# Performance work log

Measured on AMD Instinct MI355X. Metric: run time of the kernel, lower is better.

## Reference

```python
import jax, jax.numpy as jnp
import numpy as np

B, S, H = 8, 128, 768  # batch, seq_len, hidden (guide==vis)
EPS = 1e-12


def setup_inputs() -> dict:
    key = jax.random.key(0)
    ks = jax.random.split(key, 5)
    return {
        "seq_hiddens_x": jax.random.normal(ks[0], (B, S, H), jnp.float32),
        "seq_hiddens_y": jax.random.normal(ks[1], (B, S, H), jnp.float32),
        "cat_W": jax.random.normal(ks[2], (H, 2 * H), jnp.float32) * 0.02,
        "cat_b": jnp.zeros((H,), jnp.float32),
        "beta": jnp.zeros((H,), jnp.float32),
        "gamma": jnp.ones((H,), jnp.float32),
        "beta_W": jax.random.normal(ks[3], (H, H), jnp.float32) * 0.02,
        "gamma_W": jax.random.normal(ks[4], (H, H), jnp.float32) * 0.02,
    }


def reference(seq_hiddens_x, seq_hiddens_y, cat_W, cat_b, beta, gamma, beta_W, gamma_W):
    s = seq_hiddens_x.shape[1]
    # upper_reg2seq: flatten upper-triangular (i<=j) pairs, row-major
    ii, jj = np.triu_indices(s)
    guide = seq_hiddens_x[:, ii, :]    # (B, P, H)
    visible = seq_hiddens_y[:, jj, :]  # (B, P, H)

    # 'cat' branch: relu(Linear([guide; visible]))
    cat_pre = jax.nn.relu(
        jnp.einsum('bph,oh->bpo', jnp.concatenate([guide, visible], axis=-1), cat_W) + cat_b
    )

    # 'cln' branch: conditional LayerNorm(visible, cond=guide)
    # NOTE: original code uses std = (var + eps)**2 (not sqrt) -- replicated faithfully.
    b = jnp.einsum('bph,oh->bpo', guide, beta_W) + beta
    g = jnp.einsum('bph,oh->bpo', guide, gamma_W) + gamma
    mean = jnp.mean(visible, axis=-1, keepdims=True)
    cen = visible - mean
    var = jnp.mean(cen * cen, axis=-1, keepdims=True)
    std = (var + EPS) ** 2
    cln_pre = cen / std * g + b

    return (cat_pre + cln_pre) / 2.0
```

## Files before the change

kernel.cpp:

```cpp
#include <hip/hip_runtime.h>
#include <hip/hip_bf16.h>
#include <math.h>
#include <stdint.h>

#define S_LEN 128
#define H_DIM 768
#define B_DIM 8
#define NPAIR 8256
#define MROWS 1024
#define NTOT  3072
#define EPSC  1e-12f
#define CHUNK 8

typedef __bf16 bf16x8 __attribute__((ext_vector_type(8)));
typedef float  f32x4  __attribute__((ext_vector_type(4)));

static __device__ __forceinline__ unsigned short f2bf(float f) {
  union { float f; unsigned u; } a; a.f = f;
  unsigned u = a.u;
  u += 0x7fffu + ((u >> 16) & 1u);
  return (unsigned short)(u >> 16);
}
static __device__ __forceinline__ float bf2f(unsigned short s) {
  union { unsigned u; float f; } a; a.u = ((unsigned)s) << 16;
  return a.f;
}
static __device__ __forceinline__ float4 ld_bf4(const unsigned short* p) {
  ushort4 u = *(const ushort4*)p;
  float4 f; f.x = bf2f(u.x); f.y = bf2f(u.y); f.z = bf2f(u.z); f.w = bf2f(u.w);
  return f;
}

__global__ __launch_bounds__(256) void prep(const float* __restrict__ x,
                                            const float* __restrict__ y,
                                            const float* __restrict__ catW,
                                            const float* __restrict__ betaW,
                                            const float* __restrict__ gammaW,
                                            unsigned short* __restrict__ Xb,
                                            unsigned short* __restrict__ Yb,
                                            unsigned short* __restrict__ Wb,
                                            float* __restrict__ mean,
                                            float* __restrict__ inv) {
  const int bid = blockIdx.x;
  const int tid = threadIdx.x;
  if (bid < MROWS) {
    const int row = bid;
    float s = 0.f, s2 = 0.f;
    if (tid < 192) {
      const int o = tid * 4;
      float4 vx = *(const float4*)(x + (size_t)row * H_DIM + o);
      float4 vy = *(const float4*)(y + (size_t)row * H_DIM + o);
      ushort4 ox; ox.x = f2bf(vx.x); ox.y = f2bf(vx.y); ox.z = f2bf(vx.z); ox.w = f2bf(vx.w);
      ushort4 oy; oy.x = f2bf(vy.x); oy.y = f2bf(vy.y); oy.z = f2bf(vy.z); oy.w = f2bf(vy.w);
      *(ushort4*)(Xb + (size_t)row * H_DIM + o) = ox;
      *(ushort4*)(Yb + (size_t)row * H_DIM + o) = oy;
      s  = vy.x + vy.y + vy.z + vy.w;
      s2 = vy.x * vy.x + vy.y * vy.y + vy.z * vy.z + vy.w * vy.w;
    }
    for (int off = 32; off > 0; off >>= 1) { s += __shfl_down(s, off); s2 += __shfl_down(s2, off); }
    __shared__ float ls[4], ls2[4];
    if ((tid & 63) == 0) { ls[tid >> 6] = s; ls2[tid >> 6] = s2; }
    __syncthreads();
    if (tid == 0) {
      float S1 = ls[0] + ls[1] + ls[2] + ls[3];
      float S2 = ls2[0] + ls2[1] + ls2[2] + ls2[3];
      float m = S1 / H_DIM;
      float var = S2 / H_DIM - m * m;
      float st = var + EPSC;
      mean[row] = m;
      inv[row] = 1.0f / (st * st);
    }
  } else {
    int idx = (bid - MROWS) * 256 + tid;
    int e = idx * 4;
    int n = e / H_DIM, k = e % H_DIM;
    const float* src;
    if      (n < 768)  src = catW   + (size_t)n * 1536 + k;
    else if (n < 1536) src = betaW  + (size_t)(n - 768) * 768 + k;
    else if (n < 2304) src = gammaW + (size_t)(n - 1536) * 768 + k;
    else               src = catW   + (size_t)(n - 2304) * 1536 + 768 + k;
    float4 v = *(const float4*)src;
    ushort4 o; o.x = f2bf(v.x); o.y = f2bf(v.y); o.z = f2bf(v.z); o.w = f2bf(v.w);
    *(ushort4*)(Wb + e) = o;
  }
}

__device__ __forceinline__ void gload_lds16(const void* g, void* l) {
  __builtin_amdgcn_global_load_lds(
      (const __attribute__((address_space(1))) unsigned int*)(uintptr_t)g,
      (__attribute__((address_space(3))) unsigned int*)(uintptr_t)l,
      16, 0, 0);
}

__global__ __launch_bounds__(256) void gemm_bt(const unsigned short* __restrict__ Xb,
                                               const unsigned short* __restrict__ Yb,
                                               const unsigned short* __restrict__ Wb,
                                               unsigned short* __restrict__ P) {
  __shared__ unsigned short As[64 * 32];
  __shared__ unsigned short Bs[64 * 32];
  const int m0 = blockIdx.x * 64;
  const int n0 = blockIdx.y * 64;
  const unsigned short* A = (n0 < 2304) ? Xb : Yb;
  const unsigned short* Arow = A + (size_t)m0 * H_DIM;
  const unsigned short* Brow = Wb + (size_t)n0 * H_DIM;

  const int tid  = threadIdx.x;
  const int lane = tid & 63;
  const int wave = tid >> 6;
  const int wm = (wave >> 1) * 32;
  const int wn = (wave & 1) * 32;
  const int quad = lane >> 4;
  const int r    = lane & 15;

  const int ar = tid >> 2;
  const int ac = (tid & 3) * 8;

  f32x4 acc[2][2] = {};

  for (int k0 = 0; k0 < H_DIM; k0 += 32) {
    gload_lds16(Arow + (size_t)ar * H_DIM + k0 + ac, &As[tid * 8]);
    gload_lds16(Brow + (size_t)ar * H_DIM + k0 + ac, &Bs[tid * 8]);
    __syncthreads();

    bf16x8 af[2], bfr[2];
#pragma unroll
    for (int mi = 0; mi < 2; ++mi)
      af[mi] = *(const bf16x8*)&As[(wm + mi * 16 + r) * 32 + quad * 8];
#pragma unroll
    for (int ni = 0; ni < 2; ++ni)
      bfr[ni] = *(const bf16x8*)&Bs[(wn + ni * 16 + r) * 32 + quad * 8];
#pragma unroll
    for (int mi = 0; mi < 2; ++mi)
#pragma unroll
      for (int ni = 0; ni < 2; ++ni)
        acc[mi][ni] = __builtin_amdgcn_mfma_f32_16x16x32_bf16(af[mi], bfr[ni], acc[mi][ni], 0, 0, 0);
    __syncthreads();
  }

#pragma unroll
  for (int mi = 0; mi < 2; ++mi) {
#pragma unroll
    for (int ni = 0; ni < 2; ++ni) {
      const int row = m0 + wm + mi * 16 + quad * 4;
      const int col = n0 + wn + ni * 16 + r;
#pragma unroll
      for (int reg = 0; reg < 4; ++reg)
        P[(size_t)(row + reg) * NTOT + col] = f2bf(acc[mi][ni][reg]);
    }
  }
}

__global__ __launch_bounds__(192) void epilogue(const unsigned short* __restrict__ P,
                                                const float* __restrict__ Yf,
                                                const float* __restrict__ mean,
                                                const float* __restrict__ inv,
                                                const float* __restrict__ cat_b,
                                                const float* __restrict__ beta,
                                                const float* __restrict__ gamma,
                                                float* __restrict__ out) {
  const int b  = blockIdx.y;
  const int p0 = blockIdx.x * CHUNK;
  const int o  = threadIdx.x * 4;

  int i = (int)((257.0 - sqrt(257.0 * 257.0 - 8.0 * (double)p0)) * 0.5);
  if (i < 0) i = 0;
  if (i > S_LEN - 1) i = S_LEN - 1;
  while ((i + 1) * (256 - i) / 2 <= p0) ++i;
  while (i * (257 - i) / 2 > p0) --i;

  float4 cb = *(const float4*)(cat_b + o);
  float4 be = *(const float4*)(beta + o);
  float4 ga = *(const float4*)(gamma + o);

  size_t ri = (size_t)(b * S_LEN + i) * NTOT;
  float4 ax = ld_bf4(P + ri + o);
  float4 bx = ld_bf4(P + ri + 768 + o);
  float4 gx = ld_bf4(P + ri + 1536 + o);

#pragma unroll
  for (int t = 0; t < CHUNK; ++t) {
    const int p = p0 + t;
    bool moved = false;
    while ((i + 1) * (256 - i) / 2 <= p) { ++i; moved = true; }
    if (moved) {
      ri = (size_t)(b * S_LEN + i) * NTOT;
      ax = ld_bf4(P + ri + o);
      bx = ld_bf4(P + ri + 768 + o);
      gx = ld_bf4(P + ri + 1536 + o);
    }
    const int j = i + (p - i * (257 - i) / 2);
    const int rowj = b * S_LEN + j;
    float4 ay = ld_bf4(P + (size_t)rowj * NTOT + 2304 + o);
    float4 yv = *(const float4*)(Yf + (size_t)rowj * H_DIM + o);
    const float m  = mean[rowj];
    const float iv = inv[rowj];
    float4 rr;
    rr.x = 0.5f * (fmaxf(ax.x + ay.x + cb.x, 0.f) + (yv.x - m) * iv * (gx.x + ga.x) + bx.x + be.x);
    rr.y = 0.5f * (fmaxf(ax.y + ay.y + cb.y, 0.f) + (yv.y - m) * iv * (gx.y + ga.y) + bx.y + be.y);
    rr.z = 0.5f * (fmaxf(ax.z + ay.z + cb.z, 0.f) + (yv.z - m) * iv * (gx.z + ga.z) + bx.z + be.z);
    rr.w = 0.5f * (fmaxf(ax.w + ay.w + cb.w, 0.f) + (yv.w - m) * iv * (gx.w + ga.w) + bx.w + be.w);
    *(float4*)(out + ((size_t)b * NPAIR + p) * H_DIM + o) = rr;
  }
}

extern "C" void kernel_launch(void* const* d_in, const int* in_sizes, int n_in,
                              void* d_out, int out_size, void* d_ws, size_t ws_size,
                              hipStream_t stream) {
  const float* x      = (const float*)d_in[0];
  const float* y      = (const float*)d_in[1];
  const float* catW   = (const float*)d_in[2];
  const float* catb   = (const float*)d_in[3];
  const float* beta   = (const float*)d_in[4];
  const float* gamma  = (const float*)d_in[5];
  const float* betaW  = (const float*)d_in[6];
  const float* gammaW = (const float*)d_in[7];

  char* ws = (char*)d_ws;
  unsigned short* Xb   = (unsigned short*)(ws);
  unsigned short* Yb   = (unsigned short*)(ws + 1572864);
  unsigned short* Wb   = (unsigned short*)(ws + 3145728);
  unsigned short* P    = (unsigned short*)(ws + 7864320);
  float*          mean = (float*)(ws + 14155776);
  float*          inv  = (float*)(ws + 14159872);
  float*          out  = (float*)d_out;

  prep<<<MROWS + 2304, 256, 0, stream>>>(x, y, catW, betaW, gammaW, Xb, Yb, Wb, mean, inv);
  gemm_bt<<<dim3(16, 48), 256, 0, stream>>>(Xb, Yb, Wb, P);
  epilogue<<<dim3(NPAIR / CHUNK, B_DIM), 192, 0, stream>>>(P, y, mean, inv, catb, beta, gamma, out);
}
```

Before: 240.5 us.

## Double-buffer GEMM with swizzled LDS, fold biases into GEMM, precompute normalized Y

The GEMM now uses double-buffered LDS tiles with K=64 per stage and an XOR swizzle, so the next tile is fetched while the current one is computed and LDS bank conflicts are reduced. The cat and beta biases are folded into the GEMM output. The prep kernel precomputes the centered and scaled visible rows (Cy), so the epilogue no longer loads mean/inv and the biases. The epilogue also writes the large output with nontemporal stores. The trade-offs are more LDS per block and a full fp32 Cy buffer in place of two per-row scalars.

```diff
diff --git a/kernel.cpp b/kernel.cpp
--- a/kernel.cpp
+++ b/kernel.cpp
@@ -36,20 +36,24 @@
                                             const float* __restrict__ catW,
                                             const float* __restrict__ betaW,
                                             const float* __restrict__ gammaW,
+                                            const float* __restrict__ catb,
+                                            const float* __restrict__ beta,
                                             unsigned short* __restrict__ Xb,
                                             unsigned short* __restrict__ Yb,
                                             unsigned short* __restrict__ Wb,
-                                            float* __restrict__ mean,
-                                            float* __restrict__ inv) {
+                                            float* __restrict__ Cy,
+                                            float* __restrict__ bias) {
+  __shared__ float ls[4], ls2[4];
   const int bid = blockIdx.x;
   const int tid = threadIdx.x;
   if (bid < MROWS) {
     const int row = bid;
+    const int o = tid * 4;
     float s = 0.f, s2 = 0.f;
+    float4 vy = make_float4(0.f, 0.f, 0.f, 0.f);
     if (tid < 192) {
-      const int o = tid * 4;
       float4 vx = *(const float4*)(x + (size_t)row * H_DIM + o);
-      float4 vy = *(const float4*)(y + (size_t)row * H_DIM + o);
+      vy = *(const float4*)(y + (size_t)row * H_DIM + o);
       ushort4 ox; ox.x = f2bf(vx.x); ox.y = f2bf(vx.y); ox.z = f2bf(vx.z); ox.w = f2bf(vx.w);
       ushort4 oy; oy.x = f2bf(vy.x); oy.y = f2bf(vy.y); oy.z = f2bf(vy.z); oy.w = f2bf(vy.w);
       *(ushort4*)(Xb + (size_t)row * H_DIM + o) = ox;
@@ -58,19 +62,21 @@
       s2 = vy.x * vy.x + vy.y * vy.y + vy.z * vy.z + vy.w * vy.w;
     }
     for (int off = 32; off > 0; off >>= 1) { s += __shfl_down(s, off); s2 += __shfl_down(s2, off); }
-    __shared__ float ls[4], ls2[4];
     if ((tid & 63) == 0) { ls[tid >> 6] = s; ls2[tid >> 6] = s2; }
     __syncthreads();
-    if (tid == 0) {
-      float S1 = ls[0] + ls[1] + ls[2] + ls[3];
-      float S2 = ls2[0] + ls2[1] + ls2[2] + ls2[3];
-      float m = S1 / H_DIM;
-      float var = S2 / H_DIM - m * m;
-      float st = var + EPSC;
-      mean[row] = m;
-      inv[row] = 1.0f / (st * st);
-    }
-  } else {
+    const float S1 = ls[0] + ls[1] + ls[2] + ls[3];
+    const float S2 = ls2[0] + ls2[1] + ls2[2] + ls2[3];
+    const float m  = S1 / H_DIM;
+    const float var = S2 / H_DIM - m * m;
+    const float st = var + EPSC;
+    const float iv = 1.0f / (st * st);
+    if (tid < 192) {
+      float4 cy;
+      cy.x = (vy.x - m) * iv; cy.y = (vy.y - m) * iv;
+      cy.z = (vy.z - m) * iv; cy.w = (vy.w - m) * iv;
+      *(float4*)(Cy + (size_t)row * H_DIM + o) = cy;
+    }
+  } else if (bid < MROWS + 2304) {
     int idx = (bid - MROWS) * 256 + tid;
     int e = idx * 4;
     int n = e / H_DIM, k = e % H_DIM;
@@ -80,8 +86,15 @@
     else if (n < 2304) src = gammaW + (size_t)(n - 1536) * 768 + k;
     else               src = catW   + (size_t)(n - 2304) * 1536 + 768 + k;
     float4 v = *(const float4*)src;
-    ushort4 o; o.x = f2bf(v.x); o.y = f2bf(v.y); o.z = f2bf(v.z); o.w = f2bf(v.w);
-    *(ushort4*)(Wb + e) = o;
+    ushort4 o4; o4.x = f2bf(v.x); o4.y = f2bf(v.y); o4.z = f2bf(v.z); o4.w = f2bf(v.w);
+    *(ushort4*)(Wb + e) = o4;
+  } else {
+    int idx = (bid - MROWS - 2304) * 256 + tid;
+    int e = idx * 4;
+    float4 v = make_float4(0.f, 0.f, 0.f, 0.f);
+    if (e >= 768 && e < 1536) v = *(const float4*)(beta + (e - 768));
+    else if (e >= 2304)       v = *(const float4*)(catb + (e - 2304));
+    *(float4*)(bias + e) = v;
   }
 }
 
@@ -95,9 +108,10 @@
 __global__ __launch_bounds__(256) void gemm_bt(const unsigned short* __restrict__ Xb,
                                                const unsigned short* __restrict__ Yb,
                                                const unsigned short* __restrict__ Wb,
+                                               const float* __restrict__ bias,
                                                unsigned short* __restrict__ P) {
-  __shared__ unsigned short As[64 * 32];
-  __shared__ unsigned short Bs[64 * 32];
+  __shared__ unsigned short As[2][64 * 64];
+  __shared__ unsigned short Bs[2][64 * 64];
   const int m0 = blockIdx.x * 64;
   const int n0 = blockIdx.y * 64;
   const unsigned short* A = (n0 < 2304) ? Xb : Yb;
@@ -112,50 +126,76 @@
   const int quad = lane >> 4;
   const int r    = lane & 15;
 
-  const int ar = tid >> 2;
-  const int ac = (tid & 3) * 8;
+  const int q0 = tid, q1 = tid + 256;
+  const int sr0 = q0 >> 3, sc0 = (q0 & 7) ^ (sr0 & 7);
+  const int sr1 = q1 >> 3, sc1 = (q1 & 7) ^ (sr1 & 7);
+  const size_t aoff0 = (size_t)sr0 * H_DIM + sc0 * 8;
+  const size_t aoff1 = (size_t)sr1 * H_DIM + sc1 * 8;
+
+  int ard[2][2], brd[2][2];
+#pragma unroll
+  for (int ks = 0; ks < 2; ++ks)
+#pragma unroll
+    for (int mi = 0; mi < 2; ++mi) {
+      const int rowA = wm + mi * 16 + r;
+      const int rowB = wn + mi * 16 + r;
+      ard[ks][mi] = rowA * 64 + ((((ks << 2) | quad) ^ (rowA & 7)) << 3);
+      brd[ks][mi] = rowB * 64 + ((((ks << 2) | quad) ^ (rowB & 7)) << 3);
+    }
 
   f32x4 acc[2][2] = {};
 
-  for (int k0 = 0; k0 < H_DIM; k0 += 32) {
-    gload_lds16(Arow + (size_t)ar * H_DIM + k0 + ac, &As[tid * 8]);
-    gload_lds16(Brow + (size_t)ar * H_DIM + k0 + ac, &Bs[tid * 8]);
+  auto stage = [&](int buf, int k0) {
+    gload_lds16(Arow + aoff0 + k0, &As[buf][q0 * 8]);
+    gload_lds16(Arow + aoff1 + k0, &As[buf][q1 * 8]);
+    gload_lds16(Brow + aoff0 + k0, &Bs[buf][q0 * 8]);
+    gload_lds16(Brow + aoff1 + k0, &Bs[buf][q1 * 8]);
+  };
+  auto compute = [&](int buf) {
+    bf16x8 af[2][2], bfr[2][2];
+#pragma unroll
+    for (int ks = 0; ks < 2; ++ks)
+#pragma unroll
+      for (int mi = 0; mi < 2; ++mi) {
+        af[ks][mi]  = *(const bf16x8*)&As[buf][ard[ks][mi]];
+        bfr[ks][mi] = *(const bf16x8*)&Bs[buf][brd[ks][mi]];
+      }
+#pragma unroll
+    for (int ks = 0; ks < 2; ++ks)
+#pragma unroll
+      for (int mi = 0; mi < 2; ++mi)
+#pragma unroll
+        for (int ni = 0; ni < 2; ++ni)
+          acc[mi][ni] = __builtin_amdgcn_mfma_f32_16x16x32_bf16(af[ks][mi], bfr[ks][ni], acc[mi][ni], 0, 0, 0);
+  };
+
+  stage(0, 0);
+  __syncthreads();
+  int cur = 0;
+  for (int k0 = 64; k0 < H_DIM; k0 += 64) {
+    stage(cur ^ 1, k0);
+    compute(cur);
     __syncthreads();
-
-    bf16x8 af[2], bfr[2];
-#pragma unroll
-    for (int mi = 0; mi < 2; ++mi)
-      af[mi] = *(const bf16x8*)&As[(wm + mi * 16 + r) * 32 + quad * 8];
-#pragma unroll
-    for (int ni = 0; ni < 2; ++ni)
-      bfr[ni] = *(const bf16x8*)&Bs[(wn + ni * 16 + r) * 32 + quad * 8];
-#pragma unroll
-    for (int mi = 0; mi < 2; ++mi)
-#pragma unroll
-      for (int ni = 0; ni < 2; ++ni)
-        acc[mi][ni] = __builtin_amdgcn_mfma_f32_16x16x32_bf16(af[mi], bfr[ni], acc[mi][ni], 0, 0, 0);
-    __syncthreads();
-  }
-
-#pragma unroll
-  for (int mi = 0; mi < 2; ++mi) {
-#pragma unroll
-    for (int ni = 0; ni < 2; ++ni) {
+    cur ^= 1;
+  }
+  compute(cur);
+
+#pragma unroll
+  for (int ni = 0; ni < 2; ++ni) {
+    const int col = n0 + wn + ni * 16 + r;
+    const float bv = bias[col];
+#pragma unroll
+    for (int mi = 0; mi < 2; ++mi) {
       const int row = m0 + wm + mi * 16 + quad * 4;
-      const int col = n0 + wn + ni * 16 + r;
 #pragma unroll
       for (int reg = 0; reg < 4; ++reg)
-        P[(size_t)(row + reg) * NTOT + col] = f2bf(acc[mi][ni][reg]);
+        P[(size_t)(row + reg) * NTOT + col] = f2bf(acc[mi][ni][reg] + bv);
     }
   }
 }
 
 __global__ __launch_bounds__(192) void epilogue(const unsigned short* __restrict__ P,
-                                                const float* __restrict__ Yf,
-                                                const float* __restrict__ mean,
-                                                const float* __restrict__ inv,
-                                                const float* __restrict__ cat_b,
-                                                const float* __restrict__ beta,
+                                                const float* __restrict__ Cy,
                                                 const float* __restrict__ gamma,
                                                 float* __restrict__ out) {
   const int b  = blockIdx.y;
@@ -168,8 +208,6 @@
   while ((i + 1) * (256 - i) / 2 <= p0) ++i;
   while (i * (257 - i) / 2 > p0) --i;
 
-  float4 cb = *(const float4*)(cat_b + o);
-  float4 be = *(const float4*)(beta + o);
   float4 ga = *(const float4*)(gamma + o);
 
   size_t ri = (size_t)(b * S_LEN + i) * NTOT;
@@ -191,15 +229,13 @@
     const int j = i + (p - i * (257 - i) / 2);
     const int rowj = b * S_LEN + j;
     float4 ay = ld_bf4(P + (size_t)rowj * NTOT + 2304 + o);
-    float4 yv = *(const float4*)(Yf + (size_t)rowj * H_DIM + o);
-    const float m  = mean[rowj];
-    const float iv = inv[rowj];
-    float4 rr;
-    rr.x = 0.5f * (fmaxf(ax.x + ay.x + cb.x, 0.f) + (yv.x - m) * iv * (gx.x + ga.x) + bx.x + be.x);
-    rr.y = 0.5f * (fmaxf(ax.y + ay.y + cb.y, 0.f) + (yv.y - m) * iv * (gx.y + ga.y) + bx.y + be.y);
-    rr.z = 0.5f * (fmaxf(ax.z + ay.z + cb.z, 0.f) + (yv.z - m) * iv * (gx.z + ga.z) + bx.z + be.z);
-    rr.w = 0.5f * (fmaxf(ax.w + ay.w + cb.w, 0.f) + (yv.w - m) * iv * (gx.w + ga.w) + bx.w + be.w);
-    *(float4*)(out + ((size_t)b * NPAIR + p) * H_DIM + o) = rr;
+    float4 cy = *(const float4*)(Cy + (size_t)rowj * H_DIM + o);
+    f32x4 rr;
+    rr[0] = 0.5f * (fmaxf(ax.x + ay.x, 0.f) + cy.x * (gx.x + ga.x) + bx.x);
+    rr[1] = 0.5f * (fmaxf(ax.y + ay.y, 0.f) + cy.y * (gx.y + ga.y) + bx.y);
+    rr[2] = 0.5f * (fmaxf(ax.z + ay.z, 0.f) + cy.z * (gx.z + ga.z) + bx.z);
+    rr[3] = 0.5f * (fmaxf(ax.w + ay.w, 0.f) + cy.w * (gx.w + ga.w) + bx.w);
+    __builtin_nontemporal_store(rr, (f32x4*)(out + ((size_t)b * NPAIR + p) * H_DIM + o));
   }
 }
 
@@ -220,11 +256,11 @@
   unsigned short* Yb   = (unsigned short*)(ws + 1572864);
   unsigned short* Wb   = (unsigned short*)(ws + 3145728);
   unsigned short* P    = (unsigned short*)(ws + 7864320);
-  float*          mean = (float*)(ws + 14155776);
-  float*          inv  = (float*)(ws + 14159872);
+  float*          Cy   = (float*)(ws + 14155776);
+  float*          bias = (float*)(ws + 17301504);
   float*          out  = (float*)d_out;
 
-  prep<<<MROWS + 2304, 256, 0, stream>>>(x, y, catW, betaW, gammaW, Xb, Yb, Wb, mean, inv);
-  gemm_bt<<<dim3(16, 48), 256, 0, stream>>>(Xb, Yb, Wb, P);
-  epilogue<<<dim3(NPAIR / CHUNK, B_DIM), 192, 0, stream>>>(P, y, mean, inv, catb, beta, gamma, out);
-}
+  prep<<<MROWS + 2304 + 3, 256, 0, stream>>>(x, y, catW, betaW, gammaW, catb, beta, Xb, Yb, Wb, Cy, bias);
+  gemm_bt<<<dim3(16, 48), 256, 0, stream>>>(Xb, Yb, Wb, bias, P);
+  epilogue<<<dim3(NPAIR / CHUNK, B_DIM), 192, 0, stream>>>(P, Cy, gamma, out);
+}
```

Result: no change. 240.8 us (+0.1%).
